# Performance work log

Measured on AMD Instinct MI355X. Metric: run time of the kernel, lower is better.

Reference implementation:

```python
import jax, jax.numpy as jnp
import numpy as np

B, N, D, H, EF = 8, 1024, 768, 8, 4
S = D * EF          # sparse_dim = 3072
HD = S // H         # head_dim = 384
HUB_POW = 1.5
PERSIST = 0.95
EPS = 1e-6
LN_EPS = 1e-5


def setup_inputs() -> dict:
    key = jax.random.key(0)
    ks = jax.random.split(key, 8)
    s = 0.02  # weight init scale
    return {
        "x": jax.random.normal(ks[0], (B, N, D), jnp.float32),
        "memory": jax.random.normal(ks[1], (H, HD, HD), jnp.float32) * 0.01,
        "ln_g": jnp.ones((D,), jnp.float32),
        "ln_b": jnp.zeros((D,), jnp.float32),
        "w_in": jax.random.normal(ks[2], (D, 3 * S), jnp.float32) * s,
        "b_in": jnp.zeros((3 * S,), jnp.float32),
        "w_out": jax.random.normal(ks[3], (S, D), jnp.float32) * s,
        "b_out": jnp.zeros((D,), jnp.float32),
        "w_rg": jax.random.normal(ks[4], (D, H), jnp.float32) * s,
        "b_rg": jnp.zeros((H,), jnp.float32),
        "w_wg": jax.random.normal(ks[5], (D, H), jnp.float32) * s,
        "b_wg": jnp.zeros((H,), jnp.float32),
        "w_res": jax.random.normal(ks[6], (D, 1), jnp.float32) * s,
        "b_res": jnp.zeros((1,), jnp.float32),
    }


def reference(x, memory, ln_g, ln_b, w_in, b_in, w_out, b_out,
              w_rg, b_rg, w_wg, b_wg, w_res, b_res):
    residual = x
    # LayerNorm (biased variance, matching torch)
    mu = x.mean(axis=-1, keepdims=True)
    var = x.var(axis=-1, keepdims=True)
    xn = (x - mu) / jnp.sqrt(var + LN_EPS) * ln_g + ln_b

    qkv = xn @ w_in + b_in                      # [B,N,3S]
    q, k, v = jnp.split(qkv, 3, axis=-1)

    def to_heads(t):                            # [B,N,S] -> [B,H,N,hd]
        return t.reshape(B, N, H, HD).transpose(0, 2, 1, 3)

    # power-law hub feature map
    q = jnp.power(jax.nn.relu(to_heads(q)) + EPS, HUB_POW)
    k = jnp.power(jax.nn.relu(to_heads(k)) + EPS, HUB_POW)
    v = to_heads(v)
    # normalize k over the token axis
    k = k / (k.sum(axis=2, keepdims=True) + EPS)

    # per-head linear-attention state: k^T @ v -> [B,H,hd,hd]
    batch_state = jnp.einsum('bhnd,bhne->bhde', k, v)

    x_mean = xn.mean(axis=1)                    # [B,D]
    read = jax.nn.sigmoid(x_mean @ w_rg + b_rg)[:, :, None, None]   # [B,H,1,1]
    write = jax.nn.sigmoid(x_mean @ w_wg + b_wg)[:, :, None, None]  # [B,H,1,1]
    residue = jax.nn.sigmoid(xn @ w_res + b_res)                    # [B,N,1]

    # gated EMA memory update (update happens BEFORE read, as in source)
    state_mean = batch_state.mean(axis=0)       # [H,hd,hd]
    mem_new = PERSIST * memory + (1.0 - PERSIST) * write.mean(axis=0) * state_mean

    # read from updated persistent memory
    y = jnp.einsum('bhnd,bhde->bhne', q, mem_new[None] * read)
    y = y.transpose(0, 2, 1, 3).reshape(B, N, S)

    out = residue * (y @ w_out + b_out) + (1.0 - residue) * residual
    return out
```

## Files before the change

kernel.cpp:

```cpp
#include <hip/hip_runtime.h>
#include <hip/hip_bf16.h>
#include <cstdint>
#include <cstddef>


typedef __bf16 bf16_t;
typedef bf16_t bf16x4 __attribute__((ext_vector_type(4)));
typedef bf16_t bf16x8 __attribute__((ext_vector_type(8)));
typedef float f32x4 __attribute__((ext_vector_type(4)));

#define AS1 __attribute__((address_space(1)))
#define AS3 __attribute__((address_space(3)))

__device__ __forceinline__ void gemm128_bt(
    const bf16_t* __restrict__ A, int lda,
    const bf16_t* __restrict__ BT, int ldb,
    int K, int row0, int col0,
    bf16_t* As, bf16_t* Bs, f32x4 acc[4][4])
{
    const int t    = threadIdx.x;
    const int lane = t & 63;
    const int wid  = t >> 6;
    const int wr   = wid >> 1, wc = wid & 1;
    const int fr   = lane & 15;
    const int fk   = (lane >> 4) * 8;

#pragma unroll
    for (int m = 0; m < 4; ++m)
#pragma unroll
        for (int n = 0; n < 4; ++n)
            acc[m][n] = (f32x4){0.f, 0.f, 0.f, 0.f};

    const int rr = lane >> 2;
    const int rc = (lane & 3) * 8;

    for (int k0 = 0; k0 < K; k0 += 32) {
#pragma unroll
        for (int c = 0; c < 2; ++c) {
            const int q = wid * 2 + c;
            __builtin_amdgcn_global_load_lds(
                (const AS1 void*)(A + (size_t)(row0 + q * 16 + rr) * lda + (k0 + rc)),
                (AS3 void*)(As + q * 512), 16, 0, 0);
            __builtin_amdgcn_global_load_lds(
                (const AS1 void*)(BT + (size_t)(col0 + q * 16 + rr) * ldb + (k0 + rc)),
                (AS3 void*)(Bs + q * 512), 16, 0, 0);
        }
        __syncthreads();

        bf16x8 av[4], bv[4];
#pragma unroll
        for (int m = 0; m < 4; ++m)
            av[m] = *(const bf16x8*)&As[(wr * 64 + m * 16 + fr) * 32 + fk];
#pragma unroll
        for (int n = 0; n < 4; ++n)
            bv[n] = *(const bf16x8*)&Bs[(wc * 64 + n * 16 + fr) * 32 + fk];
#pragma unroll
        for (int m = 0; m < 4; ++m)
#pragma unroll
            for (int n = 0; n < 4; ++n)
                acc[m][n] = __builtin_amdgcn_mfma_f32_16x16x32_bf16(av[m], bv[n], acc[m][n], 0, 0, 0);
        __syncthreads();
    }
}

__device__ __forceinline__ void band_map(int flat, int nby, int& bx, int& by)
{
    const int xcd = flat & 7;
    const int seq = flat >> 3;
    const int bandsz = nby >> 3;
    by = xcd * bandsz + (seq % bandsz);
    bx = seq / bandsz;
}


__global__ void ktrans_w(const float* __restrict__ in, bf16_t* __restrict__ out, int R, int C)
{
    __shared__ float tl[32][33];
    const int c0 = blockIdx.x * 32, r0 = blockIdx.y * 32;
    const int tx = threadIdx.x, ty = threadIdx.y;
#pragma unroll
    for (int i = ty; i < 32; i += 8) tl[i][tx] = in[(size_t)(r0 + i) * C + c0 + tx];
    __syncthreads();
#pragma unroll
    for (int i = ty; i < 32; i += 8) out[(size_t)(c0 + i) * R + r0 + tx] = (bf16_t)tl[tx][i];
}

__device__ __forceinline__ float block_sum256(float v, float* s4)
{
#pragma unroll
    for (int off = 32; off > 0; off >>= 1) v += __shfl_down(v, off);
    const int lane = threadIdx.x & 63, w = threadIdx.x >> 6;
    if (lane == 0) s4[w] = v;
    __syncthreads();
    return s4[0] + s4[1] + s4[2] + s4[3];
}

__global__ void __launch_bounds__(256) kln(
    const float* __restrict__ x, const float* __restrict__ g, const float* __restrict__ bt,
    const float* __restrict__ w_res, const float* __restrict__ b_res,
    bf16_t* __restrict__ xn, float* __restrict__ residue)
{
    __shared__ float red[12];
    const int row = blockIdx.x;
    const float* xr = x + (size_t)row * 768;
    const int t = threadIdx.x;
    const float v0 = xr[t], v1 = xr[t + 256], v2 = xr[t + 512];
    const float ts  = block_sum256(v0 + v1 + v2, red);
    const float ts2 = block_sum256(v0 * v0 + v1 * v1 + v2 * v2, red + 4);
    const float mu  = ts * (1.f / 768.f);
    const float var = ts2 * (1.f / 768.f) - mu * mu;
    const float rs  = rsqrtf(var + 1e-5f);
    float dot = 0.f;
    {
        float xv;
        xv = (v0 - mu) * rs * g[t]       + bt[t];       xn[(size_t)row * 768 + t]       = (bf16_t)xv; dot += xv * w_res[t];
        xv = (v1 - mu) * rs * g[t + 256] + bt[t + 256]; xn[(size_t)row * 768 + t + 256] = (bf16_t)xv; dot += xv * w_res[t + 256];
        xv = (v2 - mu) * rs * g[t + 512] + bt[t + 512]; xn[(size_t)row * 768 + t + 512] = (bf16_t)xv; dot += xv * w_res[t + 512];
    }
    const float td = block_sum256(dot, red + 8);
    if (t == 0) residue[row] = 1.f / (1.f + expf(-(td + b_res[0])));
}

__global__ void kcolmean(const bf16_t* __restrict__ xn, float* __restrict__ xmean)
{
    const int b = blockIdx.x, dc = blockIdx.y, nc = blockIdx.z;
    const int d = dc * 256 + threadIdx.x;
    const bf16_t* p = xn + (size_t)(b * 1024 + nc * 128) * 768 + d;
    float s = 0.f;
#pragma unroll 4
    for (int n = 0; n < 128; ++n) s += (float)p[(size_t)n * 768];
    atomicAdd(&xmean[b * 768 + d], s);
}

__global__ void __launch_bounds__(256) kgates(
    const float* __restrict__ xmean,
    const float* __restrict__ w_rg, const float* __restrict__ b_rg,
    const float* __restrict__ w_wg, const float* __restrict__ b_wg,
    float* __restrict__ read_g, float* __restrict__ wmean)
{
    __shared__ float pr[64][4], pw[64][4], wg[64];
    const int t = threadIdx.x, grp = t >> 2, qtr = t & 3;
    const int b = grp >> 3, h = grp & 7;
    float dr = 0.f, dw = 0.f;
    for (int d = qtr * 192; d < qtr * 192 + 192; ++d) {
        const float xm = xmean[b * 768 + d] * (1.f / 1024.f);
        dr += xm * w_rg[d * 8 + h];
        dw += xm * w_wg[d * 8 + h];
    }
    pr[grp][qtr] = dr; pw[grp][qtr] = dw;
    __syncthreads();
    if (qtr == 0) {
        const float sr = pr[grp][0] + pr[grp][1] + pr[grp][2] + pr[grp][3];
        const float sw = pw[grp][0] + pw[grp][1] + pw[grp][2] + pw[grp][3];
        read_g[grp] = 1.f / (1.f + expf(-(sr + b_rg[h])));
        wg[grp]     = 1.f / (1.f + expf(-(sw + b_wg[h])));
    }
    __syncthreads();
    if (t < 8) {
        float s = 0.f;
#pragma unroll
        for (int b2 = 0; b2 < 8; ++b2) s += wg[b2 * 8 + t];
        wmean[t] = s * 0.125f;
    }
}

__global__ void __launch_bounds__(512, 2) kgemm_qkv256(
    const bf16_t* __restrict__ xnc, const bf16_t* __restrict__ w_inT,
    const float* __restrict__ b_in, const float* __restrict__ rg_c,
    bf16_t* __restrict__ qfc, bf16_t* __restrict__ kTc, bf16_t* __restrict__ vTc,
    float* __restrict__ ksum_c, int nrt )
{
    __shared__ __align__(16) bf16_t L[65536];
    const int t = threadIdx.x, lane = t & 63, wid = t >> 6;
    const int wr = wid >> 2, wc = wid & 3;
    int bx, by;
    band_map(blockIdx.y * 36 + blockIdx.x, nrt, bx, by);
    const int row0 = by * 256, col0 = bx * 256;

    f32x4 acc[8][4];
#pragma unroll
    for (int m = 0; m < 8; ++m)
#pragma unroll
        for (int n = 0; n < 4; ++n)
            acc[m][n] = (f32x4){0.f, 0.f, 0.f, 0.f};

    const int grow = 16 * wid + (lane >> 2);
    const int gcol = (lane & 3) * 8;
    const int ldst = 512 * wid + 8 * lane;

    auto stage = [&](int buf, int k0) {
        bf16_t* base = &L[buf * 32768];
#pragma unroll
        for (int op = 0; op < 2; ++op) {
            const bf16_t* src = op ? w_inT : xnc;
            const int r0 = op ? col0 : row0;
#pragma unroll
            for (int s = 0; s < 2; ++s)
#pragma unroll
                for (int j = 0; j < 2; ++j)
                    __builtin_amdgcn_global_load_lds(
                        (const AS1 void*)(src + (size_t)(r0 + 128 * j + grow) * 768 + (k0 + 32 * s + gcol)),
                        (AS3 void*)(base + op * 16384 + s * 8192 + j * 4096 + ldst),
                        16, 0, 0);
        }
    };

    const int fr = lane & 15, fo = (lane >> 4) * 8;

    stage(0, 0);
    __syncthreads();
    int cur = 0;
    for (int k0 = 0; k0 < 768; k0 += 64) {
        if (k0 + 64 < 768) stage(cur ^ 1, k0 + 64);
        const bf16_t* base = &L[cur * 32768];
#pragma unroll
        for (int s = 0; s < 2; ++s) {
            bf16x8 bv[4];
#pragma unroll
            for (int n = 0; n < 4; ++n)
                bv[n] = *(const bf16x8*)&base[16384 + s * 8192 + (wc * 64 + n * 16 + fr) * 32 + fo];
#pragma unroll
            for (int m = 0; m < 8; ++m) {
                const bf16x8 av = *(const bf16x8*)&base[s * 8192 + (wr * 128 + m * 16 + fr) * 32 + fo];
#pragma unroll
                for (int n = 0; n < 4; ++n)
                    acc[m][n] = __builtin_amdgcn_mfma_f32_16x16x32_bf16(av, bv[n], acc[m][n], 0, 0, 0);
            }
        }
        __syncthreads();
        cur ^= 1;
    }

    const int third = col0 / 3072;
    const int lb = row0 >> 10;
    if (third == 0) {
#pragma unroll
        for (int n2 = 0; n2 < 4; ++n2) {
            const int col  = col0 + wc * 64 + n2 * 16 + fr;
            const int h    = col / 384;
            const float rg = rg_c[lb * 8 + h];
            const float bias = b_in[col];
#pragma unroll
            for (int m = 0; m < 8; ++m) {
#pragma unroll
                for (int r = 0; r < 4; ++r) {
                    const int row = row0 + wr * 128 + m * 16 + (lane >> 4) * 4 + r;
                    const float v = acc[m][n2][r] + bias;
                    const float u = fmaxf(v, 0.f) + 1e-6f;
                    qfc[(size_t)row * 3072 + col] = (bf16_t)(rg * u * sqrtf(u));
                }
            }
        }
    } else {
        const int nbb = (row0 & 1023) + wr * 128 + (lane >> 4) * 4;
#pragma unroll
        for (int n2 = 0; n2 < 4; ++n2) {
            const int colg = col0 + wc * 64 + n2 * 16 + fr;
            const int coll = colg - third * 3072;
            const int h = coll / 384, d = coll % 384;
            bf16_t* dstT = ((third == 1) ? kTc : vTc) + (size_t)(lb * 8 + h) * 393216;
            const float bias = b_in[colg];
            float ksp = 0.f;
#pragma unroll
            for (int m = 0; m < 8; ++m) {
                bf16x4 pk;
#pragma unroll
                for (int r = 0; r < 4; ++r) {
                    float v = acc[m][n2][r] + bias;
                    if (third == 1) { const float u = fmaxf(v, 0.f) + 1e-6f; v = u * sqrtf(u); ksp += v; }
                    pk[r] = (bf16_t)v;
                }
                *(bf16x4*)&dstT[(size_t)d * 1024 + nbb + m * 16] = pk;
            }
            if (third == 1) atomicAdd(&ksum_c[(size_t)(lb * 8 + h) * 384 + d], ksp);
        }
    }
}

__global__ void __launch_bounds__(256) kgemm_state(
    const bf16_t* __restrict__ kTc, const bf16_t* __restrict__ vTc,
    const float* __restrict__ ksum_c, float* __restrict__ ssum)
{
    __shared__ __align__(16) bf16_t As[4096], Bs[4096];
    const int lbh = blockIdx.z, h = lbh & 7;
    const int row0 = blockIdx.y * 128, col0 = blockIdx.x * 128;
    const bf16_t* A  = kTc + (size_t)lbh * 393216;
    const bf16_t* BT = vTc + (size_t)lbh * 393216;
    f32x4 acc[4][4];
    gemm128_bt(A, 1024, BT, 1024, 1024, row0, col0, As, Bs, acc);

    const int lane = threadIdx.x & 63, wid = threadIdx.x >> 6;
    const int wr = wid >> 1, wc = wid & 1;
    float* ss = ssum + (size_t)h * 147456;
#pragma unroll
    for (int m = 0; m < 4; ++m) {
#pragma unroll
        for (int r = 0; r < 4; ++r) {
            const int d = row0 + wr * 64 + m * 16 + (lane >> 4) * 4 + r;
            const float sc = 1.f / (ksum_c[(size_t)lbh * 384 + d] + 1e-6f);
#pragma unroll
            for (int n = 0; n < 4; ++n) {
                const int e = col0 + wc * 64 + n * 16 + (lane & 15);
                atomicAdd(&ss[(size_t)d * 384 + e], acc[m][n][r] * sc);
            }
        }
    }
}

__global__ void kmemupd_ew(const float* __restrict__ mem, const float* __restrict__ ssum,
                           const float* __restrict__ wmean, bf16_t* __restrict__ mem_new)
{
    const int idx = blockIdx.x * 256 + threadIdx.x;
    const int h = idx / 147456;
    const float wm = wmean[h] * (0.05f / 8.f);
    mem_new[idx] = (bf16_t)(0.95f * mem[idx] + wm * ssum[idx]);
}

__global__ void __launch_bounds__(256) kgemm_G(
    const bf16_t* __restrict__ w_outT, const bf16_t* __restrict__ mem_new,
    bf16_t* __restrict__ GT)
{
    __shared__ __align__(16) bf16_t As[4096], Bs[4096];
    const int h = blockIdx.z;
    const int row0 = blockIdx.y * 128, col0 = blockIdx.x * 128;
    f32x4 acc[4][4];
    gemm128_bt(w_outT + h * 384, 3072, mem_new + (size_t)h * 147456, 384,
               384, row0, col0, As, Bs, acc);

    const int lane = threadIdx.x & 63, wid = threadIdx.x >> 6;
    const int wr = wid >> 1, wc = wid & 1;
#pragma unroll
    for (int m = 0; m < 4; ++m) {
#pragma unroll
        for (int n = 0; n < 4; ++n) {
            const int d = col0 + wc * 64 + n * 16 + (lane & 15);
#pragma unroll
            for (int r = 0; r < 4; ++r) {
                const int c = row0 + wr * 64 + m * 16 + (lane >> 4) * 4 + r;
                GT[(size_t)c * 3072 + h * 384 + d] = (bf16_t)acc[m][n][r];
            }
        }
    }
}

__global__ void __launch_bounds__(256) kgemm_out(
    const bf16_t* __restrict__ qf, const bf16_t* __restrict__ GT,
    const float* __restrict__ b_out, const float* __restrict__ residue,
    const float* __restrict__ x, float* __restrict__ out)
{
    __shared__ __align__(16) bf16_t As[4096], Bs[4096];
    int bx, by;
    band_map(blockIdx.y * 6 + blockIdx.x, 64, bx, by);
    const int row0 = by * 128, col0 = bx * 128;
    f32x4 acc[4][4];
    gemm128_bt(qf, 3072, GT, 3072, 3072, row0, col0, As, Bs, acc);

    const int lane = threadIdx.x & 63, wid = threadIdx.x >> 6;
    const int wr = wid >> 1, wc = wid & 1;
#pragma unroll
    for (int m = 0; m < 4; ++m) {
#pragma unroll
        for (int n = 0; n < 4; ++n) {
            const int col = col0 + wc * 64 + n * 16 + (lane & 15);
            const float bias = b_out[col];
#pragma unroll
            for (int r = 0; r < 4; ++r) {
                const int row = row0 + wr * 64 + m * 16 + (lane >> 4) * 4 + r;
                const float v = acc[m][n][r] + bias;
                const float rr = residue[row];
                out[(size_t)row * 768 + col] = rr * v + (1.f - rr) * x[(size_t)row * 768 + col];
            }
        }
    }
}

extern "C" void kernel_launch(void* const* d_in, const int* in_sizes, int n_in,
                              void* d_out, int out_size, void* d_ws, size_t ws_size,
                              hipStream_t stream)
{
    (void)in_sizes; (void)n_in; (void)out_size;
    const float* x     = (const float*)d_in[0];
    const float* mem   = (const float*)d_in[1];
    const float* ln_g  = (const float*)d_in[2];
    const float* ln_b  = (const float*)d_in[3];
    const float* w_in  = (const float*)d_in[4];
    const float* b_in  = (const float*)d_in[5];
    const float* w_out = (const float*)d_in[6];
    const float* b_out = (const float*)d_in[7];
    const float* w_rg  = (const float*)d_in[8];
    const float* b_rg  = (const float*)d_in[9];
    const float* w_wg  = (const float*)d_in[10];
    const float* b_wg  = (const float*)d_in[11];
    const float* w_res = (const float*)d_in[12];
    const float* b_res = (const float*)d_in[13];
    float* out = (float*)d_out;

    auto total_for = [&](int c) -> size_t {
        size_t o = 0;
        auto a = [&](size_t b) { o += (b + 255) & ~(size_t)255; };
        a(50331648);
        a(14155776); a(12582912);
        a((size_t)c * 6291456);
        a((size_t)c * 6291456);
        a(4718592); a(4718592); a(2359296);
        a(32768); a(24576); a(98304); a(256); a(256);
        return o;
    };
    int CHUNK = 0;
    for (int c = 8; c >= 2; c >>= 1) if (total_for(c) <= ws_size) { CHUNK = c; break; }
    if (CHUNK == 0) return;

    char* ws = (char*)d_ws;
    size_t off = 0;
    auto alloc = [&](size_t bytes) -> char* {
        char* p = ws + off; off += (bytes + 255) & ~(size_t)255; return p;
    };
    bf16_t* qf      = (bf16_t*)alloc(50331648);
    bf16_t* w_inT   = (bf16_t*)alloc(14155776);
    bf16_t* GT      = w_inT;
    bf16_t* xn      = (bf16_t*)alloc(12582912);
    bf16_t* kTc     = (bf16_t*)alloc((size_t)CHUNK * 6291456);
    bf16_t* vTc     = (bf16_t*)alloc((size_t)CHUNK * 6291456);
    bf16_t* w_outT  = (bf16_t*)alloc(4718592);
    float*  ssum    = (float*) alloc(4718592);
    bf16_t* mem_new = (bf16_t*)alloc(2359296);
    float*  residue = (float*) alloc(32768);
    float*  xmean   = (float*) alloc(24576);
    float*  ksum    = (float*) alloc(98304);
    float*  read_g  = (float*) alloc(256);
    float*  wmean   = (float*) alloc(256);

    hipMemsetAsync(xmean, 0, 24576, stream);
    hipMemsetAsync(ksum,  0, 98304, stream);
    hipMemsetAsync(ssum,  0, 4718592, stream);

    ktrans_w<<<dim3(288, 24), dim3(32, 8), 0, stream>>>(w_in, w_inT, 768, 9216);
    ktrans_w<<<dim3(24, 96), dim3(32, 8), 0, stream>>>(w_out, w_outT, 3072, 768);
    kln<<<8192, 256, 0, stream>>>(x, ln_g, ln_b, w_res, b_res, xn, residue);
    kcolmean<<<dim3(8, 3, 8), 256, 0, stream>>>(xn, xmean);
    kgates<<<1, 256, 0, stream>>>(xmean, w_rg, b_rg, w_wg, b_wg, read_g, wmean);

    const int NC = 8 / CHUNK;
    for (int c = 0; c < NC; ++c) {
        const int b0 = c * CHUNK;
        kgemm_qkv256<<<dim3(36, CHUNK * 4), 512, 0, stream>>>(
            xn + (size_t)b0 * 1024 * 768, w_inT, b_in, read_g + b0 * 8,
            qf + (size_t)b0 * 1024 * 3072, kTc, vTc,
            ksum + (size_t)b0 * 8 * 384, CHUNK * 4);
        kgemm_state<<<dim3(3, 3, CHUNK * 8), 256, 0, stream>>>(
            kTc, vTc, ksum + (size_t)b0 * 8 * 384, ssum);
    }

    kmemupd_ew<<<4608, 256, 0, stream>>>(mem, ssum, wmean, mem_new);
    kgemm_G<<<dim3(3, 6, 8), 256, 0, stream>>>(w_outT, mem_new, GT);
    kgemm_out<<<dim3(6, 64), 256, 0, stream>>>(qf, GT, b_out, residue, x, out);
}
```

Baseline: 375.6 us.

## Restructure QKV GEMM main loop into phased ping-pong with swizzled LDS

Rewrites the 256x256 QKV projection main loop so that it runs in four barrier-separated phases. Each phase loads a quarter of the LDS fragments into registers, issues the next tile's global-to-LDS prefetch in pieces, and runs a block of MFMAs at raised wave priority. The LDS layout is changed to an XOR-swizzled per-row slot to avoid bank conflicts, and the loop is split into separate stage_piece calls per operand half. The intent is to overlap memory traffic with MFMA work and reduce LDS conflicts, at the cost of more barriers per iteration and tighter ordering assumptions.

```diff
diff --git a/kernel.cpp b/kernel.cpp
--- a/kernel.cpp
+++ b/kernel.cpp
@@ -11,6 +11,10 @@
 
 #define AS1 __attribute__((address_space(1)))
 #define AS3 __attribute__((address_space(3)))
+
+#define SYNC_B do { __builtin_amdgcn_sched_barrier(0); \
+                    __builtin_amdgcn_s_barrier(); \
+                    __builtin_amdgcn_sched_barrier(0); } while (0)
 
 __device__ __forceinline__ void gemm128_bt(
     const bf16_t* __restrict__ A, int lda,
@@ -184,51 +188,90 @@
         for (int n = 0; n < 4; ++n)
             acc[m][n] = (f32x4){0.f, 0.f, 0.f, 0.f};
 
-    const int grow = 16 * wid + (lane >> 2);
-    const int gcol = (lane & 3) * 8;
-    const int ldst = 512 * wid + 8 * lane;
-
-    auto stage = [&](int buf, int k0) {
-        bf16_t* base = &L[buf * 32768];
-#pragma unroll
-        for (int op = 0; op < 2; ++op) {
-            const bf16_t* src = op ? w_inT : xnc;
-            const int r0 = op ? col0 : row0;
-#pragma unroll
-            for (int s = 0; s < 2; ++s)
-#pragma unroll
-                for (int j = 0; j < 2; ++j)
-                    __builtin_amdgcn_global_load_lds(
-                        (const AS1 void*)(src + (size_t)(r0 + 128 * j + grow) * 768 + (k0 + 32 * s + gcol)),
-                        (AS3 void*)(base + op * 16384 + s * 8192 + j * 4096 + ldst),
-                        16, 0, 0);
-        }
+    const int sgrow = t >> 2;
+    const int sgcol = (((t & 3) ^ ((t >> 3) & 3)) * 8);
+    const int xslot = (((lane >> 4) ^ ((lane >> 1) & 3))) * 8;
+    const int fr = lane & 15;
+
+    auto stage_piece = [&](int op, int rh, int kt2) {
+        const bf16_t* src = op ? w_inT : xnc;
+        const int r0 = (op ? col0 : row0) + rh * 128;
+        const size_t srow = (size_t)(r0 + sgrow) * 768 + kt2 * 64 + sgcol;
+        bf16_t* dst = &L[op * 32768 + (kt2 & 1) * 16384 + rh * 8192 + wid * 512];
+#pragma unroll
+        for (int s = 0; s < 2; ++s)
+            __builtin_amdgcn_global_load_lds(
+                (const AS1 void*)(src + srow + s * 32),
+                (AS3 void*)(dst + s * 4096), 16, 0, 0);
     };
 
-    const int fr = lane & 15, fo = (lane >> 4) * 8;
-
-    stage(0, 0);
-    __syncthreads();
-    int cur = 0;
-    for (int k0 = 0; k0 < 768; k0 += 64) {
-        if (k0 + 64 < 768) stage(cur ^ 1, k0 + 64);
-        const bf16_t* base = &L[cur * 32768];
-#pragma unroll
-        for (int s = 0; s < 2; ++s) {
-            bf16x8 bv[4];
+    stage_piece(0, 0, 0); stage_piece(0, 1, 0);
+    stage_piece(1, 0, 0); stage_piece(1, 1, 0);
+    asm volatile("s_waitcnt vmcnt(0)" ::: "memory");
+    SYNC_B;
+
+    const int NT = 12;
+    for (int kt = 0; kt < NT; ++kt) {
+        const int kb = (kt & 1) * 16384;
+        const bf16_t* Ab = &L[kb + wr * 8192];
+        const bf16_t* Bb = &L[32768 + kb + (wc >> 1) * 8192 + (wc & 1) * 2048];
+        const bool pre = (kt + 1 < NT);
+        bf16x8 av[4], bv[4];
+
+#pragma unroll
+        for (int n = 0; n < 4; ++n) bv[n] = *(const bf16x8*)&Bb[(n * 16 + fr) * 32 + xslot];
+#pragma unroll
+        for (int m = 0; m < 4; ++m) av[m] = *(const bf16x8*)&Ab[(m * 16 + fr) * 32 + xslot];
+        if (pre) { stage_piece(0, 0, kt + 1); stage_piece(0, 1, kt + 1); }
+        SYNC_B;
+        __builtin_amdgcn_s_setprio(1);
+#pragma unroll
+        for (int m = 0; m < 4; ++m)
 #pragma unroll
             for (int n = 0; n < 4; ++n)
-                bv[n] = *(const bf16x8*)&base[16384 + s * 8192 + (wc * 64 + n * 16 + fr) * 32 + fo];
-#pragma unroll
-            for (int m = 0; m < 8; ++m) {
-                const bf16x8 av = *(const bf16x8*)&base[s * 8192 + (wr * 128 + m * 16 + fr) * 32 + fo];
-#pragma unroll
-                for (int n = 0; n < 4; ++n)
-                    acc[m][n] = __builtin_amdgcn_mfma_f32_16x16x32_bf16(av, bv[n], acc[m][n], 0, 0, 0);
-            }
-        }
-        __syncthreads();
-        cur ^= 1;
+                acc[m][n] = __builtin_amdgcn_mfma_f32_16x16x32_bf16(av[m], bv[n], acc[m][n], 0, 0, 0);
+        __builtin_amdgcn_s_setprio(0);
+        SYNC_B;
+
+#pragma unroll
+        for (int m = 0; m < 4; ++m) av[m] = *(const bf16x8*)&Ab[((m + 4) * 16 + fr) * 32 + xslot];
+        if (pre) { stage_piece(1, 0, kt + 1); stage_piece(1, 1, kt + 1); }
+        SYNC_B;
+        __builtin_amdgcn_s_setprio(1);
+#pragma unroll
+        for (int m = 0; m < 4; ++m)
+#pragma unroll
+            for (int n = 0; n < 4; ++n)
+                acc[m + 4][n] = __builtin_amdgcn_mfma_f32_16x16x32_bf16(av[m], bv[n], acc[m + 4][n], 0, 0, 0);
+        __builtin_amdgcn_s_setprio(0);
+        SYNC_B;
+
+#pragma unroll
+        for (int n = 0; n < 4; ++n) bv[n] = *(const bf16x8*)&Bb[4096 + (n * 16 + fr) * 32 + xslot];
+#pragma unroll
+        for (int m = 0; m < 4; ++m) av[m] = *(const bf16x8*)&Ab[4096 + (m * 16 + fr) * 32 + xslot];
+        SYNC_B;
+        __builtin_amdgcn_s_setprio(1);
+#pragma unroll
+        for (int m = 0; m < 4; ++m)
+#pragma unroll
+            for (int n = 0; n < 4; ++n)
+                acc[m][n] = __builtin_amdgcn_mfma_f32_16x16x32_bf16(av[m], bv[n], acc[m][n], 0, 0, 0);
+        __builtin_amdgcn_s_setprio(0);
+        SYNC_B;
+
+#pragma unroll
+        for (int m = 0; m < 4; ++m) av[m] = *(const bf16x8*)&Ab[4096 + ((m + 4) * 16 + fr) * 32 + xslot];
+        SYNC_B;
+        __builtin_amdgcn_s_setprio(1);
+#pragma unroll
+        for (int m = 0; m < 4; ++m)
+#pragma unroll
+            for (int n = 0; n < 4; ++n)
+                acc[m + 4][n] = __builtin_amdgcn_mfma_f32_16x16x32_bf16(av[m], bv[n], acc[m + 4][n], 0, 0, 0);
+        __builtin_amdgcn_s_setprio(0);
+        asm volatile("s_waitcnt vmcnt(0)" ::: "memory");
+        SYNC_B;
     }
 
     const int third = col0 / 3072;
```

New measurement: 379.6 us. No clear change (+1.1%).

## Use 256x256 tiles for output GEMM and per-batch state slots without atomics

Applied to the files above, without the earlier changes.

The 256x256 double-buffered MFMA mainloop from the QKV GEMM is factored into a shared helper, and the output GEMM moves from 128x128 tiles with 256 threads to 256x256 tiles with 512 threads. Each tile now reuses more data per LDS load, but the grid shrinks from 384 to 96 blocks, which may leave compute units idle. Separately, when the workspace is large enough, the state GEMM writes each batch's k^T v into its own slot instead of using float atomics, and the memory-update kernel sums the 8 slots. This drops the atomic contention and the memset, at the cost of extra workspace and extra reads in the update kernel.

```diff
diff --git a/kernel.cpp b/kernel.cpp
--- a/kernel.cpp
+++ b/kernel.cpp
@@ -60,6 +60,70 @@
             for (int n = 0; n < 4; ++n)
                 acc[m][n] = __builtin_amdgcn_mfma_f32_16x16x32_bf16(av[m], bv[n], acc[m][n], 0, 0, 0);
         __syncthreads();
+    }
+}
+
+__device__ __forceinline__ void gemm256_bt(
+    const bf16_t* __restrict__ A, int lda,
+    const bf16_t* __restrict__ BT, int ldb,
+    int K, int row0, int col0,
+    bf16_t* L, f32x4 acc[8][4])
+{
+    const int t = threadIdx.x, lane = t & 63, wid = t >> 6;
+    const int wr = wid >> 2, wc = wid & 3;
+
+#pragma unroll
+    for (int m = 0; m < 8; ++m)
+#pragma unroll
+        for (int n = 0; n < 4; ++n)
+            acc[m][n] = (f32x4){0.f, 0.f, 0.f, 0.f};
+
+    const int grow = 16 * wid + (lane >> 2);
+    const int gcol = (lane & 3) * 8;
+    const int ldst = 512 * wid + 8 * lane;
+
+    auto stage = [&](int buf, int k0) {
+        bf16_t* base = &L[buf * 32768];
+#pragma unroll
+        for (int op = 0; op < 2; ++op) {
+            const bf16_t* src = op ? BT : A;
+            const int ld  = op ? ldb : lda;
+            const int r0  = op ? col0 : row0;
+#pragma unroll
+            for (int s = 0; s < 2; ++s)
+#pragma unroll
+                for (int j = 0; j < 2; ++j)
+                    __builtin_amdgcn_global_load_lds(
+                        (const AS1 void*)(src + (size_t)(r0 + 128 * j + grow) * ld + (k0 + 32 * s + gcol)),
+                        (AS3 void*)(base + op * 16384 + s * 8192 + j * 4096 + ldst),
+                        16, 0, 0);
+        }
+    };
+
+    const int fr = lane & 15, fo = (lane >> 4) * 8;
+
+    stage(0, 0);
+    __syncthreads();
+    int cur = 0;
+    for (int k0 = 0; k0 < K; k0 += 64) {
+        if (k0 + 64 < K) stage(cur ^ 1, k0 + 64);
+        const bf16_t* base = &L[cur * 32768];
+#pragma unroll
+        for (int s = 0; s < 2; ++s) {
+            bf16x8 bv[4];
+#pragma unroll
+            for (int n = 0; n < 4; ++n)
+                bv[n] = *(const bf16x8*)&base[16384 + s * 8192 + (wc * 64 + n * 16 + fr) * 32 + fo];
+#pragma unroll
+            for (int m = 0; m < 8; ++m) {
+                const bf16x8 av = *(const bf16x8*)&base[s * 8192 + (wr * 128 + m * 16 + fr) * 32 + fo];
+#pragma unroll
+                for (int n = 0; n < 4; ++n)
+                    acc[m][n] = __builtin_amdgcn_mfma_f32_16x16x32_bf16(av, bv[n], acc[m][n], 0, 0, 0);
+            }
+        }
+        __syncthreads();
+        cur ^= 1;
     }
 }
 
@@ -171,66 +235,16 @@
     float* __restrict__ ksum_c, int nrt )
 {
     __shared__ __align__(16) bf16_t L[65536];
-    const int t = threadIdx.x, lane = t & 63, wid = t >> 6;
+    const int lane = threadIdx.x & 63, wid = threadIdx.x >> 6;
     const int wr = wid >> 2, wc = wid & 3;
     int bx, by;
     band_map(blockIdx.y * 36 + blockIdx.x, nrt, bx, by);
     const int row0 = by * 256, col0 = bx * 256;
 
     f32x4 acc[8][4];
-#pragma unroll
-    for (int m = 0; m < 8; ++m)
-#pragma unroll
-        for (int n = 0; n < 4; ++n)
-            acc[m][n] = (f32x4){0.f, 0.f, 0.f, 0.f};
-
-    const int grow = 16 * wid + (lane >> 2);
-    const int gcol = (lane & 3) * 8;
-    const int ldst = 512 * wid + 8 * lane;
-
-    auto stage = [&](int buf, int k0) {
-        bf16_t* base = &L[buf * 32768];
-#pragma unroll
-        for (int op = 0; op < 2; ++op) {
-            const bf16_t* src = op ? w_inT : xnc;
-            const int r0 = op ? col0 : row0;
-#pragma unroll
-            for (int s = 0; s < 2; ++s)
-#pragma unroll
-                for (int j = 0; j < 2; ++j)
-                    __builtin_amdgcn_global_load_lds(
-                        (const AS1 void*)(src + (size_t)(r0 + 128 * j + grow) * 768 + (k0 + 32 * s + gcol)),
-                        (AS3 void*)(base + op * 16384 + s * 8192 + j * 4096 + ldst),
-                        16, 0, 0);
-        }
-    };
-
-    const int fr = lane & 15, fo = (lane >> 4) * 8;
-
-    stage(0, 0);
-    __syncthreads();
-    int cur = 0;
-    for (int k0 = 0; k0 < 768; k0 += 64) {
-        if (k0 + 64 < 768) stage(cur ^ 1, k0 + 64);
-        const bf16_t* base = &L[cur * 32768];
-#pragma unroll
-        for (int s = 0; s < 2; ++s) {
-            bf16x8 bv[4];
-#pragma unroll
-            for (int n = 0; n < 4; ++n)
-                bv[n] = *(const bf16x8*)&base[16384 + s * 8192 + (wc * 64 + n * 16 + fr) * 32 + fo];
-#pragma unroll
-            for (int m = 0; m < 8; ++m) {
-                const bf16x8 av = *(const bf16x8*)&base[s * 8192 + (wr * 128 + m * 16 + fr) * 32 + fo];
-#pragma unroll
-                for (int n = 0; n < 4; ++n)
-                    acc[m][n] = __builtin_amdgcn_mfma_f32_16x16x32_bf16(av, bv[n], acc[m][n], 0, 0, 0);
-            }
-        }
-        __syncthreads();
-        cur ^= 1;
-    }
-
+    gemm256_bt(xnc, 768, w_inT, 768, 768, row0, col0, L, acc);
+
+    const int fr = lane & 15;
     const int third = col0 / 3072;
     const int lb = row0 >> 10;
     if (third == 0) {
@@ -279,10 +293,10 @@
 
 __global__ void __launch_bounds__(256) kgemm_state(
     const bf16_t* __restrict__ kTc, const bf16_t* __restrict__ vTc,
-    const float* __restrict__ ksum_c, float* __restrict__ ssum)
+    const float* __restrict__ ksum_c, float* __restrict__ ssb, int nslot)
 {
     __shared__ __align__(16) bf16_t As[4096], Bs[4096];
-    const int lbh = blockIdx.z, h = lbh & 7;
+    const int lbh = blockIdx.z, lb = lbh >> 3, h = lbh & 7;
     const int row0 = blockIdx.y * 128, col0 = blockIdx.x * 128;
     const bf16_t* A  = kTc + (size_t)lbh * 393216;
     const bf16_t* BT = vTc + (size_t)lbh * 393216;
@@ -291,7 +305,7 @@
 
     const int lane = threadIdx.x & 63, wid = threadIdx.x >> 6;
     const int wr = wid >> 1, wc = wid & 1;
-    float* ss = ssum + (size_t)h * 147456;
+    float* ss = ssb + ((nslot == 8) ? (size_t)lb * 1179648 : 0) + (size_t)h * 147456;
 #pragma unroll
     for (int m = 0; m < 4; ++m) {
 #pragma unroll
@@ -301,19 +315,29 @@
 #pragma unroll
             for (int n = 0; n < 4; ++n) {
                 const int e = col0 + wc * 64 + n * 16 + (lane & 15);
-                atomicAdd(&ss[(size_t)d * 384 + e], acc[m][n][r] * sc);
-            }
-        }
-    }
-}
-
-__global__ void kmemupd_ew(const float* __restrict__ mem, const float* __restrict__ ssum,
-                           const float* __restrict__ wmean, bf16_t* __restrict__ mem_new)
+                const float v = acc[m][n][r] * sc;
+                if (nslot == 8) ss[(size_t)d * 384 + e] = v;
+                else            atomicAdd(&ss[(size_t)d * 384 + e], v);
+            }
+        }
+    }
+}
+
+__global__ void kmemupd_ew(const float* __restrict__ mem, const float* __restrict__ ssum8,
+                           const float* __restrict__ wmean, bf16_t* __restrict__ mem_new,
+                           int nslot)
 {
     const int idx = blockIdx.x * 256 + threadIdx.x;
     const int h = idx / 147456;
     const float wm = wmean[h] * (0.05f / 8.f);
-    mem_new[idx] = (bf16_t)(0.95f * mem[idx] + wm * ssum[idx]);
+    float s = 0.f;
+    if (nslot == 8) {
+#pragma unroll
+        for (int b = 0; b < 8; ++b) s += ssum8[(size_t)b * 1179648 + idx];
+    } else {
+        s = ssum8[idx];
+    }
+    mem_new[idx] = (bf16_t)(0.95f * mem[idx] + wm * s);
 }
 
 __global__ void __launch_bounds__(256) kgemm_G(
@@ -343,30 +367,32 @@
     }
 }
 
-__global__ void __launch_bounds__(256) kgemm_out(
+__global__ void __launch_bounds__(512, 2) kgemm_out256(
     const bf16_t* __restrict__ qf, const bf16_t* __restrict__ GT,
     const float* __restrict__ b_out, const float* __restrict__ residue,
     const float* __restrict__ x, float* __restrict__ out)
 {
-    __shared__ __align__(16) bf16_t As[4096], Bs[4096];
+    __shared__ __align__(16) bf16_t L[65536];
+    const int lane = threadIdx.x & 63, wid = threadIdx.x >> 6;
+    const int wr = wid >> 2, wc = wid & 3;
     int bx, by;
-    band_map(blockIdx.y * 6 + blockIdx.x, 64, bx, by);
-    const int row0 = by * 128, col0 = bx * 128;
-    f32x4 acc[4][4];
-    gemm128_bt(qf, 3072, GT, 3072, 3072, row0, col0, As, Bs, acc);
-
-    const int lane = threadIdx.x & 63, wid = threadIdx.x >> 6;
-    const int wr = wid >> 1, wc = wid & 1;
-#pragma unroll
-    for (int m = 0; m < 4; ++m) {
-#pragma unroll
-        for (int n = 0; n < 4; ++n) {
-            const int col = col0 + wc * 64 + n * 16 + (lane & 15);
-            const float bias = b_out[col];
+    band_map(blockIdx.y * 3 + blockIdx.x, 32, bx, by);
+    const int row0 = by * 256, col0 = bx * 256;
+
+    f32x4 acc[8][4];
+    gemm256_bt(qf, 3072, GT, 3072, 3072, row0, col0, L, acc);
+
+    const int fr = lane & 15;
+#pragma unroll
+    for (int n2 = 0; n2 < 4; ++n2) {
+        const int col = col0 + wc * 64 + n2 * 16 + fr;
+        const float bias = b_out[col];
+#pragma unroll
+        for (int m = 0; m < 8; ++m) {
 #pragma unroll
             for (int r = 0; r < 4; ++r) {
-                const int row = row0 + wr * 64 + m * 16 + (lane >> 4) * 4 + r;
-                const float v = acc[m][n][r] + bias;
+                const int row = row0 + wr * 128 + m * 16 + (lane >> 4) * 4 + r;
+                const float v = acc[m][n2][r] + bias;
                 const float rr = residue[row];
                 out[(size_t)row * 768 + col] = rr * v + (1.f - rr) * x[(size_t)row * 768 + col];
             }
@@ -395,19 +421,27 @@
     const float* b_res = (const float*)d_in[13];
     float* out = (float*)d_out;
 
-    auto total_for = [&](int c) -> size_t {
+    auto total_for = [&](int c, int ns) -> size_t {
         size_t o = 0;
         auto a = [&](size_t b) { o += (b + 255) & ~(size_t)255; };
         a(50331648);
         a(14155776); a(12582912);
         a((size_t)c * 6291456);
         a((size_t)c * 6291456);
-        a(4718592); a(4718592); a(2359296);
+        a(4718592);
+        a((size_t)ns * 4718592);
+        a(2359296);
         a(32768); a(24576); a(98304); a(256); a(256);
         return o;
     };
-    int CHUNK = 0;
-    for (int c = 8; c >= 2; c >>= 1) if (total_for(c) <= ws_size) { CHUNK = c; break; }
+    int CHUNK = 0, NSLOT = 1;
+    {
+        const int cand[6][2] = {{8,8},{8,1},{4,8},{4,1},{2,8},{2,1}};
+        for (int i = 0; i < 6; ++i)
+            if (total_for(cand[i][0], cand[i][1]) <= ws_size) {
+                CHUNK = cand[i][0]; NSLOT = cand[i][1]; break;
+            }
+    }
     if (CHUNK == 0) return;
 
     char* ws = (char*)d_ws;
@@ -422,7 +456,7 @@
     bf16_t* kTc     = (bf16_t*)alloc((size_t)CHUNK * 6291456);
     bf16_t* vTc     = (bf16_t*)alloc((size_t)CHUNK * 6291456);
     bf16_t* w_outT  = (bf16_t*)alloc(4718592);
-    float*  ssum    = (float*) alloc(4718592);
+    float*  ssum8   = (float*) alloc((size_t)NSLOT * 4718592);
     bf16_t* mem_new = (bf16_t*)alloc(2359296);
     float*  residue = (float*) alloc(32768);
     float*  xmean   = (float*) alloc(24576);
@@ -432,7 +466,7 @@
 
     hipMemsetAsync(xmean, 0, 24576, stream);
     hipMemsetAsync(ksum,  0, 98304, stream);
-    hipMemsetAsync(ssum,  0, 4718592, stream);
+    if (NSLOT == 1) hipMemsetAsync(ssum8, 0, 4718592, stream);
 
     ktrans_w<<<dim3(288, 24), dim3(32, 8), 0, stream>>>(w_in, w_inT, 768, 9216);
     ktrans_w<<<dim3(24, 96), dim3(32, 8), 0, stream>>>(w_out, w_outT, 3072, 768);
@@ -448,10 +482,11 @@
             qf + (size_t)b0 * 1024 * 3072, kTc, vTc,
             ksum + (size_t)b0 * 8 * 384, CHUNK * 4);
         kgemm_state<<<dim3(3, 3, CHUNK * 8), 256, 0, stream>>>(
-            kTc, vTc, ksum + (size_t)b0 * 8 * 384, ssum);
-    }
-
-    kmemupd_ew<<<4608, 256, 0, stream>>>(mem, ssum, wmean, mem_new);
+            kTc, vTc, ksum + (size_t)b0 * 8 * 384,
+            ssum8 + ((NSLOT == 8) ? (size_t)b0 * 1179648 : 0), NSLOT);
+    }
+
+    kmemupd_ew<<<4608, 256, 0, stream>>>(mem, ssum8, wmean, mem_new, NSLOT);
     kgemm_G<<<dim3(3, 6, 8), 256, 0, stream>>>(w_outT, mem_new, GT);
-    kgemm_out<<<dim3(6, 64), 256, 0, stream>>>(qf, GT, b_out, residue, x, out);
-}
+    kgemm_out256<<<dim3(3, 32), 512, 0, stream>>>(qf, GT, b_out, residue, x, out);
+}
```

Measured after the change: 421.2 us. +12.2%, slower.
